# Performance work log

Hardware: AMD Instinct MI355X
Metric: run time of the kernel (lower is better)

The kernel has to match this reference:

```python
import jax, jax.numpy as jnp
import numpy as np
from jax import lax

N_QUBITS = 8
N_BLOCKS = 5

_H = jnp.array([[1.0, 1.0], [1.0, -1.0]], dtype=jnp.complex64) / np.sqrt(2.0).astype(np.float32)
# torchquantum PauliY.diagonalizing_gates = [Z, S, H] applied in order -> matrix H @ S @ Z = H @ diag(1, -1j)
_YROT = _H @ jnp.diag(jnp.array([1.0, -1j], dtype=jnp.complex64))


def apply_gate(st, U, wires):
    # st: [N, 2, 2, ..., 2] (n_qubits trailing axes); U: [2^k, 2^k]
    k = len(wires)
    axes = [w + 1 for w in wires]
    s = jnp.moveaxis(st, axes, list(range(1, k + 1)))
    shp = s.shape
    s = s.reshape(shp[0], 2 ** k, -1)
    s = jnp.einsum('ij,bjr->bir', U, s)
    return jnp.moveaxis(s.reshape(shp), list(range(1, k + 1)), axes)


def u3_mat(th, ph, lam):
    c = jnp.cos(0.5 * th).astype(jnp.complex64)
    s = jnp.sin(0.5 * th).astype(jnp.complex64)
    el = jnp.exp(1j * lam)
    ep = jnp.exp(1j * ph)
    return jnp.stack([jnp.stack([c, -el * s]), jnp.stack([ep * s, ep * el * c])])


def cu3_mat(th, ph, lam):
    M = jnp.eye(4, dtype=jnp.complex64)
    return M.at[2:, 2:].set(u3_mat(th, ph, lam))


def z_expvals(st):
    # <Z_w> for every wire from marginal probabilities
    n = st.ndim - 1
    mag = st.real ** 2 + st.imag ** 2
    outs = []
    for w in range(n):
        axes = tuple(a for a in range(1, n + 1) if a != w + 1)
        p = mag.sum(axes)  # [N, 2]
        outs.append(p[:, 0] - p[:, 1])
    return jnp.stack(outs, axis=1)


def quantum_conv(x, conv_w, conv_b, u3_params, cu3_params, fc_w, fc_b):
    n = N_QUBITS
    B, C, H, W = x.shape
    y = lax.conv_general_dilated(x, conv_w, (1, 1), 'SAME',
                                 dimension_numbers=('NCHW', 'OIHW', 'NCHW'))
    y = y + conv_b[None, :, None, None]
    ang = y.transpose(0, 2, 3, 1).reshape(-1, n)  # [B*H*W, n_qubits]
    Npx = ang.shape[0]
    # RY(theta)|0> encoding: product state of [cos(t/2), sin(t/2)] per wire
    c = jnp.cos(0.5 * ang)
    s = jnp.sin(0.5 * ang)
    st = jnp.stack([c[:, 0], s[:, 0]], axis=1).astype(jnp.complex64)
    for w in range(1, n):
        q = jnp.stack([c[:, w], s[:, w]], axis=1).astype(jnp.complex64)
        st = (st[:, :, None] * q[:, None, :]).reshape(Npx, -1)
    st = st.reshape((Npx,) + (2,) * n)
    # U3CU3Layer0: per block, U3 on each wire then circular CU3 ring
    for b in range(N_BLOCKS):
        for w in range(n):
            st = apply_gate(st, u3_mat(u3_params[b, w, 0], u3_params[b, w, 1], u3_params[b, w, 2]), [w])
        for w in range(n):
            st = apply_gate(st, cu3_mat(cu3_params[b, w, 0], cu3_params[b, w, 1], cu3_params[b, w, 2]), [w, (w + 1) % n])
    # MeasureAll(Z), then MeasureAll(X) and MeasureAll(Y) which MUTATE the device
    # state with their diagonalizing gates (torchquantum semantics)
    mz = z_expvals(st)
    for w in range(n):
        st = apply_gate(st, _H, [w])
    mx = z_expvals(st)
    for w in range(n):
        st = apply_gate(st, _YROT, [w])
    my = z_expvals(st)
    meas = jnp.concatenate([mz, mx, my], axis=1)  # [B*H*W, 3*n]
    out = meas @ fc_w.T + fc_b
    return out.reshape(B, H, W, -1).transpose(0, 3, 1, 2)


def setup_inputs() -> dict:
    key = jax.random.key(0)
    ks = jax.random.split(key, 7)
    n, cin, cout = N_QUBITS, 16, 32
    x = jax.random.normal(ks[0], (4, cin, 64, 64), dtype=jnp.float32)
    conv_w = jax.random.normal(ks[1], (n, cin, 3, 3), dtype=jnp.float32) / np.sqrt(cin * 9)
    conv_b = jax.random.normal(ks[2], (n,), dtype=jnp.float32) * 0.01
    u3_params = jax.random.uniform(ks[3], (N_BLOCKS, n, 3), dtype=jnp.float32, minval=-np.pi, maxval=np.pi)
    cu3_params = jax.random.uniform(ks[4], (N_BLOCKS, n, 3), dtype=jnp.float32, minval=-np.pi, maxval=np.pi)
    fc_w = jax.random.normal(ks[5], (cout, 3 * n), dtype=jnp.float32) / np.sqrt(3 * n)
    fc_b = jax.random.normal(ks[6], (cout,), dtype=jnp.float32) * 0.01
    return {'x': x, 'conv_w': conv_w, 'conv_b': conv_b, 'u3_params': u3_params,
            'cu3_params': cu3_params, 'fc_w': fc_w, 'fc_b': fc_b}


def reference(x, conv_w, conv_b, u3_params, cu3_params, fc_w, fc_b):
    return quantum_conv(x, conv_w, conv_b, u3_params, cu3_params, fc_w, fc_b)
```

## Files before the change

### kernel.cpp

```cpp
#include <hip/hip_runtime.h>

typedef float v2f __attribute__((ext_vector_type(2)));

template<int C>
__device__ __forceinline__ float dppmov(float x) {
  return __int_as_float(__builtin_amdgcn_update_dpp(0, __float_as_int(x), C, 0xF, 0xF, true));
}
template<int IMM>
__device__ __forceinline__ float dswz(float x) {
  return __int_as_float(__builtin_amdgcn_ds_swizzle(__float_as_int(x), IMM));
}
__device__ __forceinline__ float bperm(float x, int a) {
  return __int_as_float(__builtin_amdgcn_ds_bpermute(a, __float_as_int(x)));
}
template<int M>
__device__ __forceinline__ float bfly(float x) {
  if constexpr (M == 1)      return dppmov<0xB1>(x);
  else if constexpr (M == 2) return dppmov<0x4E>(x);
  else if constexpr (M == 3) return dppmov<0x1B>(x);
  else if constexpr (M == 8) return dppmov<0x128>(x);
  else                       return dswz<0x101F>(x);
}
template<int M>
__device__ __forceinline__ v2f bfly2(v2f v) {
  v2f o; o.x = bfly<M>(v.x); o.y = bfly<M>(v.y); return o;
}
__device__ __forceinline__ v2f sp(float s) { v2f v; v.x = s; v.y = s; return v; }
__device__ __forceinline__ v2f vfma(v2f a, v2f b, v2f c) {
  return __builtin_elementwise_fma(a, b, c);
}

template<int M, int CM>
__device__ __forceinline__ void crossG(v2f Sr[16], v2f Si[16],
    const float* __restrict__ g, int lane) {
  const bool hi = (lane & M) != 0;
  const bool ct = (lane & CM) != 0;
  float f0r = hi ? g[6]  : g[0],  f0i = hi ? g[7]  : g[1];
  float g0r = hi ? g[4]  : g[2],  g0i = hi ? g[5]  : g[3];
  float f1r = hi ? g[14] : g[8],  f1i = hi ? g[15] : g[9];
  float g1r = hi ? g[12] : g[10], g1i = hi ? g[13] : g[11];
  float fr = ct ? f1r : f0r, fi = ct ? f1i : f0i;
  float gr = ct ? g1r : g0r, gi = ct ? g1i : g0i;
  v2f vfr = sp(fr), vfi = sp(fi), vgr = sp(gr), vgi = sp(gi);
  v2f vfiN = sp(-fi), vgiN = sp(-gi);
#pragma unroll
  for (int r = 0; r < 16; ++r) {
    v2f pR = bfly2<M>(Sr[r]);
    v2f pI = bfly2<M>(Si[r]);
    v2f nR = vfma(vgiN, pI, vfma(vgr, pR, vfma(vfiN, Si[r], vfr * Sr[r])));
    v2f nI = vfma(vgi,  pR, vfma(vgr, pI, vfma(vfi,  Sr[r], vfr * Si[r])));
    Sr[r] = nR; Si[r] = nI;
  }
}

__device__ __forceinline__ void mixP(v2f& x0r, v2f& x0i, v2f& x1r, v2f& x1i,
    float m0r, float m0i, float m1r, float m1i,
    float m2r, float m2i, float m3r, float m3i) {
  v2f n0r = vfma(sp(-m1i), x1i, vfma(sp(m1r), x1r, vfma(sp(-m0i), x0i, sp(m0r) * x0r)));
  v2f n0i = vfma(sp( m1i), x1r, vfma(sp(m1r), x1i, vfma(sp( m0i), x0r, sp(m0r) * x0i)));
  v2f n1r = vfma(sp(-m3i), x1i, vfma(sp(m3r), x1r, vfma(sp(-m2i), x0i, sp(m2r) * x0r)));
  v2f n1i = vfma(sp( m3i), x1r, vfma(sp(m3r), x1i, vfma(sp( m2i), x0r, sp(m2r) * x0i)));
  x0r = n0r; x0i = n0i; x1r = n1r; x1i = n1i;
}

__device__ __forceinline__ void f4N(v2f Sr[16], v2f Si[16],
    const float* __restrict__ g, int lane) {
  const bool ct = (lane & 1) != 0;
  float m[8];
#pragma unroll
  for (int jj = 0; jj < 8; ++jj) m[jj] = ct ? g[8 + jj] : g[jj];
#pragma unroll
  for (int r = 0; r < 8; ++r)
    mixP(Sr[r], Si[r], Sr[r + 8], Si[r + 8],
         m[0], m[1], m[2], m[3], m[4], m[5], m[6], m[7]);
}
__device__ __forceinline__ void f5N(v2f Sr[16], v2f Si[16],
    const float* __restrict__ g) {
#pragma unroll
  for (int r = 0; r < 4; ++r)
    mixP(Sr[r], Si[r], Sr[r + 4], Si[r + 4],
         g[0], g[1], g[2], g[3], g[4], g[5], g[6], g[7]);
#pragma unroll
  for (int r = 8; r < 12; ++r)
    mixP(Sr[r], Si[r], Sr[r + 4], Si[r + 4],
         g[8], g[9], g[10], g[11], g[12], g[13], g[14], g[15]);
}
__device__ __forceinline__ void f67N(v2f Sr[16], v2f Si[16],
    const float* __restrict__ T) {
#pragma unroll
  for (int qd = 0; qd < 4; ++qd) {
    const int B = qd * 4;
    const float* __restrict__ M = T + (qd & 1) * 32;
    v2f ar0 = Sr[B+0], ai0 = Si[B+0], ar1 = Sr[B+1], ai1 = Si[B+1];
    v2f ar2 = Sr[B+2], ai2 = Si[B+2], ar3 = Sr[B+3], ai3 = Si[B+3];
#pragma unroll
    for (int rp = 0; rp < 4; ++rp) {
      const float* __restrict__ Mr = M + rp * 8;
      v2f nR = sp(Mr[0]) * ar0;
      nR = vfma(sp(-Mr[1]), ai0, nR);
      nR = vfma(sp( Mr[2]), ar1, nR);
      nR = vfma(sp(-Mr[3]), ai1, nR);
      nR = vfma(sp( Mr[4]), ar2, nR);
      nR = vfma(sp(-Mr[5]), ai2, nR);
      nR = vfma(sp( Mr[6]), ar3, nR);
      nR = vfma(sp(-Mr[7]), ai3, nR);
      v2f nI = sp(Mr[1]) * ar0;
      nI = vfma(sp(Mr[0]), ai0, nI);
      nI = vfma(sp(Mr[3]), ar1, nI);
      nI = vfma(sp(Mr[2]), ai1, nI);
      nI = vfma(sp(Mr[5]), ar2, nI);
      nI = vfma(sp(Mr[4]), ai2, nI);
      nI = vfma(sp(Mr[7]), ar3, nI);
      nI = vfma(sp(Mr[6]), ai3, nI);
      Sr[B + rp] = nR; Si[B + rp] = nI;
    }
  }
}
__device__ __forceinline__ void f8pN(v2f Sr[16], v2f Si[16],
    const float* __restrict__ g, int lane) {
  const bool hi = (lane & 8) != 0;
  float fr[2], fi[2], gr[2], gi[2];
  fr[0] = hi ? g[6]  : g[0];  fi[0] = hi ? g[7]  : g[1];
  gr[0] = hi ? g[4]  : g[2];  gi[0] = hi ? g[5]  : g[3];
  fr[1] = hi ? g[14] : g[8];  fi[1] = hi ? g[15] : g[9];
  gr[1] = hi ? g[12] : g[10]; gi[1] = hi ? g[13] : g[11];
#pragma unroll
  for (int r = 0; r < 16; ++r) {
    const int m = r & 1;
    v2f pR = bfly2<8>(Sr[r]);
    v2f pI = bfly2<8>(Si[r]);
    v2f nR = vfma(sp(-gi[m]), pI, vfma(sp(gr[m]), pR, vfma(sp(-fi[m]), Si[r], sp(fr[m]) * Sr[r])));
    v2f nI = vfma(sp( gi[m]), pR, vfma(sp(gr[m]), pI, vfma(sp( fi[m]), Sr[r], sp(fr[m]) * Si[r])));
    Sr[r] = nR; Si[r] = nI;
  }
}
__device__ __forceinline__ void f8N(v2f Sr[16], v2f Si[16],
    const float* __restrict__ g, int lane) {
  const bool hi = (lane & 8) != 0;
  const float fr = hi ? g[6] : g[0], fi = hi ? g[7] : g[1];
  const float gr = hi ? g[4] : g[2], gi = hi ? g[5] : g[3];
#pragma unroll
  for (int r = 1; r < 16; r += 2) {
    v2f pR = bfly2<8>(Sr[r]);
    v2f pI = bfly2<8>(Si[r]);
    v2f nR = vfma(sp(-gi), pI, vfma(sp(gr), pR, vfma(sp(-fi), Si[r], sp(fr) * Sr[r])));
    v2f nI = vfma(sp( gi), pR, vfma(sp(gr), pI, vfma(sp( fi), Sr[r], sp(fr) * Si[r])));
    Sr[r] = nR; Si[r] = nI;
  }
}

template<int M>
__device__ __forceinline__ void crossO(const v2f Sr[16], const v2f Si[16],
                                       v2f& re, v2f& im) {
  v2f r = sp(0.0f), i = sp(0.0f);
#pragma unroll
  for (int k = 0; k < 16; ++k) {
    v2f pr = bfly2<M>(Sr[k]);
    v2f pi = bfly2<M>(Si[k]);
    r = vfma(Sr[k], pr, r);
    r = vfma(Si[k], pi, r);
    i = vfma(Si[k], pr, i);
    i = vfma(-Sr[k], pi, i);
  }
  re = r; im = i;
}

__device__ __forceinline__ void mm2(const float* A, const float* B, float* D) {
  D[0] = A[0]*B[0] - A[1]*B[1] + A[2]*B[4] - A[3]*B[5];
  D[1] = A[0]*B[1] + A[1]*B[0] + A[2]*B[5] + A[3]*B[4];
  D[2] = A[0]*B[2] - A[1]*B[3] + A[2]*B[6] - A[3]*B[7];
  D[3] = A[0]*B[3] + A[1]*B[2] + A[2]*B[7] + A[3]*B[6];
  D[4] = A[4]*B[0] - A[5]*B[1] + A[6]*B[4] - A[7]*B[5];
  D[5] = A[4]*B[1] + A[5]*B[0] + A[6]*B[5] + A[7]*B[4];
  D[6] = A[4]*B[2] - A[5]*B[3] + A[6]*B[6] - A[7]*B[7];
  D[7] = A[4]*B[3] + A[5]*B[2] + A[6]*B[7] + A[7]*B[6];
}
__device__ __forceinline__ void u3fill(const float* src, float* o) {
  float th = src[0], ph = src[1], lam = src[2];
  float c = cosf(0.5f * th), s = sinf(0.5f * th);
  float cl = cosf(lam), sl = sinf(lam);
  float cp = cosf(ph), spv = sinf(ph);
  float cpl = cosf(ph + lam), spl = sinf(ph + lam);
  o[0] = c;        o[1] = 0.0f;
  o[2] = -cl * s;  o[3] = -sl * s;
  o[4] = cp * s;   o[5] = spv * s;
  o[6] = cpl * c;  o[7] = spl * c;
}

__global__ __launch_bounds__(256) void qprep_kernel(
    const float* __restrict__ u3p, const float* __restrict__ cu3p,
    const float* __restrict__ fcw, float* __restrict__ ws) {
  __shared__ float Us[40][8];
  __shared__ float Cs[40][8];
  __shared__ float Gs[640];
  const int t = threadIdx.x;
  if (t < 40) u3fill(u3p + t * 3, Us[t]);
  if (t >= 64 && t < 104) u3fill(cu3p + (t - 64) * 3, Cs[t - 64]);
  __syncthreads();
  if (t == 0) {
#pragma unroll
    for (int j = 0; j < 8; ++j) Gs[j] = Us[0][j];
  } else if (t < 36) {
    int j = t - 1, b = j / 7, k = j % 7;
    float* dst = Gs + 8 + b * 112 + k * 16;
    const float* U = Us[b * 8 + k + 1];
    const float* C = Cs[b * 8 + k];
#pragma unroll
    for (int u = 0; u < 8; ++u) dst[u] = U[u];
    mm2(C, U, dst + 8);
  } else if (t < 40) {
    int b = t - 36;
    float* dst = Gs + 568 + b * 16;
    const float* U = Us[(b + 1) * 8];
    const float* C = Cs[b * 8 + 7];
#pragma unroll
    for (int u = 0; u < 8; ++u) dst[u] = U[u];
    mm2(U, C, dst + 8);
  } else if (t == 40) {
#pragma unroll
    for (int j = 0; j < 8; ++j) Gs[632 + j] = Cs[39][j];
  }
  __syncthreads();
  if (t >= 64 && t < 104) {
    int u = t - 64;
    int b = u >> 3, idx = u & 7;
    int ct = idx >> 2, rp = idx & 3;
    const float* M6 = Gs + 8 + b * 112 + 80 + ct * 8;
    int b1p = rp >> 1, b0p = rp & 1;
    const float* M7 = Gs + 8 + b * 112 + 96 + b1p * 8;
    float* dst = ws + 1536 + b * 64 + ct * 32 + rp * 8;
#pragma unroll
    for (int c = 0; c < 4; ++c) {
      int b1 = c >> 1, b0 = c & 1;
      float a_r = M6[(b1p * 2 + b1) * 2], a_i = M6[(b1p * 2 + b1) * 2 + 1];
      float b_r = M7[(b0p * 2 + b0) * 2], b_i = M7[(b0p * 2 + b0) * 2 + 1];
      dst[c * 2]     = a_r * b_r - a_i * b_i;
      dst[c * 2 + 1] = a_r * b_i + a_i * b_r;
    }
  }
  for (int i = t; i < 32 * 28; i += 256) {
    int ch = i / 28, u = i - ch * 28;
    float v = 0.0f;
    if (u < 24) {
      float sc = (u >= 8 && (u & 7) >= 4) ? 2.0f : 1.0f;
      v = fcw[ch * 24 + u] * sc;
    }
    ws[640 + i] = v;
  }
  for (int i = t; i < 640; i += 256) ws[i] = Gs[i];
}

__global__ __launch_bounds__(256) void qconv_kernel(
    const float* __restrict__ x, const float* __restrict__ cw,
    const float* __restrict__ cb, const float* __restrict__ fcb,
    const float* __restrict__ wsc, float* __restrict__ out) {
  __shared__ float FCWs[32 * 28];
  for (int i = threadIdx.x; i < 32 * 28; i += 256) FCWs[i] = wsc[640 + i];
  __syncthreads();

  const int lane = threadIdx.x & 63;
  const int wid = __builtin_amdgcn_readfirstlane(
      (int)((blockIdx.x * blockDim.x + threadIdx.x) >> 6));
  const int p0 = wid * 8;
  const int q = lane & 15;

  float ang;
  {
    const int px = lane >> 3;
    const int oc = lane & 7;
    const int p  = p0 + px;
    const int b  = p >> 12;
    const int hh = (p >> 6) & 63;
    const int wim = p & 63;
    float acc = cb[oc];
#pragma unroll 4
    for (int ic = 0; ic < 16; ++ic) {
      const float* wp = cw + (oc * 16 + ic) * 9;
      const float* xp = x + (b * 16 + ic) * 4096;
#pragma unroll
      for (int kh = 0; kh < 3; ++kh) {
        int ih = hh + kh - 1;
        bool rok = (unsigned)ih < 64u;
        int ihc = rok ? ih : 0;
#pragma unroll
        for (int kw = 0; kw < 3; ++kw) {
          int iw = wim + kw - 1;
          bool ok = rok && ((unsigned)iw < 64u);
          int iwc = ((unsigned)iw < 64u) ? iw : 0;
          float xv = xp[ihc * 64 + iwc];
          acc = fmaf(ok ? xv : 0.0f, wp[kh * 3 + kw], acc);
        }
      }
    }
    ang = acc;
  }

  v2f Sr[16], Si[16];
  {
    const int gb = (lane & 48) << 2;
    float aA[8], aB[8];
#pragma unroll
    for (int w = 0; w < 8; ++w) {
      aA[w] = bperm(ang, gb + (w << 2));
      aB[w] = bperm(ang, gb + ((8 + w) << 2));
    }
    float cA[8], sA[8], cB[8], sB[8];
#pragma unroll
    for (int w = 0; w < 8; ++w) {
      __sincosf(0.5f * aA[w], &sA[w], &cA[w]);
      __sincosf(0.5f * aB[w], &sB[w], &cB[w]);
    }
    v2f c0; c0.x = cA[0]; c0.y = cB[0];
    v2f s0; s0.x = sA[0]; s0.y = sB[0];
    v2f c0r = vfma(sp(wsc[2]), s0, sp(wsc[0]) * c0);
    v2f c0i = vfma(sp(wsc[3]), s0, sp(wsc[1]) * c0);
    v2f s0r = vfma(sp(wsc[6]), s0, sp(wsc[4]) * c0);
    v2f s0i = vfma(sp(wsc[7]), s0, sp(wsc[5]) * c0);
    const bool w0 = (q & 8) != 0;
    v2f selR = w0 ? s0r : c0r;
    v2f selI = w0 ? s0i : c0i;
    float fA = ((q & 4) ? sA[1] : cA[1]) * ((q & 2) ? sA[2] : cA[2])
             * ((q & 1) ? sA[3] : cA[3]);
    float fB = ((q & 4) ? sB[1] : cB[1]) * ((q & 2) ? sB[2] : cB[2])
             * ((q & 1) ? sB[3] : cB[3]);
    v2f uu[4], vv[4];
    uu[0].x = cA[6]*cA[7]; uu[1].x = cA[6]*sA[7];
    uu[2].x = sA[6]*cA[7]; uu[3].x = sA[6]*sA[7];
    uu[0].y = cB[6]*cB[7]; uu[1].y = cB[6]*sB[7];
    uu[2].y = sB[6]*cB[7]; uu[3].y = sB[6]*sB[7];
    float vA0 = fA * cA[4], vA1 = fA * sA[4];
    float vB0 = fB * cB[4], vB1 = fB * sB[4];
    vv[0].x = vA0*cA[5]; vv[1].x = vA0*sA[5];
    vv[2].x = vA1*cA[5]; vv[3].x = vA1*sA[5];
    vv[0].y = vB0*cB[5]; vv[1].y = vB0*sB[5];
    vv[2].y = vB1*cB[5]; vv[3].y = vB1*sB[5];
#pragma unroll
    for (int r = 0; r < 16; ++r) {
      v2f base = vv[r >> 2] * uu[r & 3];
      Sr[r] = selR * base;
      Si[r] = selI * base;
    }
  }

  for (int b = 0; b < 5; ++b) {
    const float* __restrict__ base = wsc + 8 + b * 112;
    crossG<4, 8>(Sr, Si, base + 0, lane);
    crossG<2, 4>(Sr, Si, base + 16, lane);
    crossG<1, 2>(Sr, Si, base + 32, lane);
    f4N(Sr, Si, base + 48, lane);
    f5N(Sr, Si, base + 64);
    f67N(Sr, Si, wsc + 1536 + b * 64);
    if (b < 4) f8pN(Sr, Si, wsc + 568 + b * 16, lane);
  }
  f8N(Sr, Si, wsc + 632, lane);

  float sg[4];
  sg[0] = (q & 8) ? -1.0f : 1.0f;
  sg[1] = (q & 4) ? -1.0f : 1.0f;
  sg[2] = (q & 2) ? -1.0f : 1.0f;
  sg[3] = (q & 1) ? -1.0f : 1.0f;

  v2f PT[24];
  {
    v2f re0, im0, re1, im1, re2, im2, re3, im3;
    crossO<8>(Sr, Si, re0, im0);
    crossO<4>(Sr, Si, re1, im1);
    crossO<2>(Sr, Si, re2, im2);
    crossO<1>(Sr, Si, re3, im3);
    PT[8]  = re0; PT[9]  = re1; PT[10] = re2; PT[11] = re3;
    PT[16] = sp(sg[0]) * im0; PT[17] = sp(sg[1]) * im1;
    PT[18] = sp(sg[2]) * im2; PT[19] = sp(sg[3]) * im3;

    v2f P[16];
#pragma unroll
    for (int r = 0; r < 16; ++r) P[r] = vfma(Si[r], Si[r], Sr[r] * Sr[r]);
    v2f t01[8];
#pragma unroll
    for (int k = 0; k < 8; ++k) t01[k] = P[2*k] + P[2*k+1];
    v2f q0 = t01[0] + t01[1], q1 = t01[2] + t01[3];
    v2f q2 = t01[4] + t01[5], q3 = t01[6] + t01[7];
    v2f h0 = q0 + q1, h1 = q2 + q3;
    v2f p  = h0 + h1;
    PT[4] = h0 - h1;
    PT[5] = (q0 - q1) + (q2 - q3);
    PT[6] = (t01[0]-t01[1]) + (t01[2]-t01[3])
          + (t01[4]-t01[5]) + (t01[6]-t01[7]);
    PT[7] = (P[0]-P[1]) + (P[2]-P[3]) + (P[4]-P[5]) + (P[6]-P[7])
          + (P[8]-P[9]) + (P[10]-P[11]) + (P[12]-P[13]) + (P[14]-P[15]);
    PT[0] = sp(sg[0]) * p; PT[1] = sp(sg[1]) * p;
    PT[2] = sp(sg[2]) * p; PT[3] = sp(sg[3]) * p;

    v2f re, im;
    re = sp(0.0f); im = sp(0.0f);
#pragma unroll
    for (int r = 0; r < 8; ++r) {
      re = vfma(Sr[r], Sr[r+8], re); re = vfma(Si[r], Si[r+8], re);
      im = vfma(Si[r], Sr[r+8], im); im = vfma(-Sr[r], Si[r+8], im);
    }
    PT[12] = re; PT[20] = im;
    re = sp(0.0f); im = sp(0.0f);
#pragma unroll
    for (int t = 0; t < 8; ++t) {
      const int lo = (t & 3) + (t >> 2) * 8;
      re = vfma(Sr[lo], Sr[lo+4], re); re = vfma(Si[lo], Si[lo+4], re);
      im = vfma(Si[lo], Sr[lo+4], im); im = vfma(-Sr[lo], Si[lo+4], im);
    }
    PT[13] = re; PT[21] = im;
    re = sp(0.0f); im = sp(0.0f);
#pragma unroll
    for (int t = 0; t < 8; ++t) {
      const int lo = (t & 1) + (t >> 1) * 4;
      re = vfma(Sr[lo], Sr[lo+2], re); re = vfma(Si[lo], Si[lo+2], re);
      im = vfma(Si[lo], Sr[lo+2], im); im = vfma(-Sr[lo], Si[lo+2], im);
    }
    PT[14] = re; PT[22] = im;
    re = sp(0.0f); im = sp(0.0f);
#pragma unroll
    for (int t = 0; t < 8; ++t) {
      const int lo = 2 * t;
      re = vfma(Sr[lo], Sr[lo+1], re); re = vfma(Si[lo], Si[lo+1], re);
      im = vfma(Si[lo], Sr[lo+1], im); im = vfma(-Sr[lo], Si[lo+1], im);
    }
    PT[15] = re; PT[23] = im;
  }

  const int j = q & 7;
  const bool isB = (q & 8) != 0;
  float mm[24];
#pragma unroll
  for (int t = 0; t < 24; ++t) {
    v2f v = PT[t] + bfly2<8>(PT[t]);
    float s = isB ? v.y : v.x;
    s += bfly<1>(s);
    s += bfly<2>(s);
    s += bfly<4>(s);
    mm[t] = s;
  }

  const int g = lane >> 4;
  const int p = p0 + 2 * g + (isB ? 1 : 0);
  const int ob = (p >> 12) * 131072 + (p & 4095);
#pragma unroll
  for (int k = 0; k < 4; ++k) {
    const int ch = 4 * j + k;
    const float* wr = FCWs + ch * 28;
    float acc = fcb[ch];
#pragma unroll
    for (int u = 0; u < 24; ++u) acc = fmaf(mm[u], wr[u], acc);
    out[ob + ch * 4096] = acc;
  }
}

extern "C" void kernel_launch(void* const* d_in, const int* in_sizes, int n_in,
                              void* d_out, int out_size, void* d_ws, size_t ws_size,
                              hipStream_t stream) {
  const float* x      = (const float*)d_in[0];
  const float* conv_w = (const float*)d_in[1];
  const float* conv_b = (const float*)d_in[2];
  const float* u3p    = (const float*)d_in[3];
  const float* cu3p   = (const float*)d_in[4];
  const float* fcw    = (const float*)d_in[5];
  const float* fcb    = (const float*)d_in[6];
  float* out = (float*)d_out;
  float* ws  = (float*)d_ws;

  qprep_kernel<<<1, 256, 0, stream>>>(u3p, cu3p, fcw, ws);
  qconv_kernel<<<512, 256, 0, stream>>>(x, conv_w, conv_b, fcb, ws, out);
}
```

Baseline: 112.7 us.

## Fuse gate-prep kernel into main kernel and read gate matrices from LDS

```diff
diff --git a/kernel.cpp b/kernel.cpp
--- a/kernel.cpp
+++ b/kernel.cpp
@@ -5,10 +5,6 @@
 template<int C>
 __device__ __forceinline__ float dppmov(float x) {
   return __int_as_float(__builtin_amdgcn_update_dpp(0, __float_as_int(x), C, 0xF, 0xF, true));
-}
-template<int IMM>
-__device__ __forceinline__ float dswz(float x) {
-  return __int_as_float(__builtin_amdgcn_ds_swizzle(__float_as_int(x), IMM));
 }
 __device__ __forceinline__ float bperm(float x, int a) {
   return __int_as_float(__builtin_amdgcn_ds_bpermute(a, __float_as_int(x)));
@@ -19,7 +15,7 @@
   else if constexpr (M == 2) return dppmov<0x4E>(x);
   else if constexpr (M == 3) return dppmov<0x1B>(x);
   else if constexpr (M == 8) return dppmov<0x128>(x);
-  else                       return dswz<0x101F>(x);
+  else                       return dppmov<0x1B>(dppmov<0x141>(x));
 }
 template<int M>
 __device__ __forceinline__ v2f bfly2(v2f v) {
@@ -32,7 +28,7 @@
 
 template<int M, int CM>
 __device__ __forceinline__ void crossG(v2f Sr[16], v2f Si[16],
-    const float* __restrict__ g, int lane) {
+    const float* g, int lane) {
   const bool hi = (lane & M) != 0;
   const bool ct = (lane & CM) != 0;
   float f0r = hi ? g[6]  : g[0],  f0i = hi ? g[7]  : g[1];
@@ -64,7 +60,7 @@
 }
 
 __device__ __forceinline__ void f4N(v2f Sr[16], v2f Si[16],
-    const float* __restrict__ g, int lane) {
+    const float* g, int lane) {
   const bool ct = (lane & 1) != 0;
   float m[8];
 #pragma unroll
@@ -74,8 +70,7 @@
     mixP(Sr[r], Si[r], Sr[r + 8], Si[r + 8],
          m[0], m[1], m[2], m[3], m[4], m[5], m[6], m[7]);
 }
-__device__ __forceinline__ void f5N(v2f Sr[16], v2f Si[16],
-    const float* __restrict__ g) {
+__device__ __forceinline__ void f5N(v2f Sr[16], v2f Si[16], const float* g) {
 #pragma unroll
   for (int r = 0; r < 4; ++r)
     mixP(Sr[r], Si[r], Sr[r + 4], Si[r + 4],
@@ -85,17 +80,16 @@
     mixP(Sr[r], Si[r], Sr[r + 4], Si[r + 4],
          g[8], g[9], g[10], g[11], g[12], g[13], g[14], g[15]);
 }
-__device__ __forceinline__ void f67N(v2f Sr[16], v2f Si[16],
-    const float* __restrict__ T) {
+__device__ __forceinline__ void f67N(v2f Sr[16], v2f Si[16], const float* T) {
 #pragma unroll
   for (int qd = 0; qd < 4; ++qd) {
     const int B = qd * 4;
-    const float* __restrict__ M = T + (qd & 1) * 32;
+    const float* M = T + (qd & 1) * 32;
     v2f ar0 = Sr[B+0], ai0 = Si[B+0], ar1 = Sr[B+1], ai1 = Si[B+1];
     v2f ar2 = Sr[B+2], ai2 = Si[B+2], ar3 = Sr[B+3], ai3 = Si[B+3];
 #pragma unroll
     for (int rp = 0; rp < 4; ++rp) {
-      const float* __restrict__ Mr = M + rp * 8;
+      const float* Mr = M + rp * 8;
       v2f nR = sp(Mr[0]) * ar0;
       nR = vfma(sp(-Mr[1]), ai0, nR);
       nR = vfma(sp( Mr[2]), ar1, nR);
@@ -117,7 +111,7 @@
   }
 }
 __device__ __forceinline__ void f8pN(v2f Sr[16], v2f Si[16],
-    const float* __restrict__ g, int lane) {
+    const float* g, int lane) {
   const bool hi = (lane & 8) != 0;
   float fr[2], fi[2], gr[2], gi[2];
   fr[0] = hi ? g[6]  : g[0];  fi[0] = hi ? g[7]  : g[1];
@@ -135,7 +129,7 @@
   }
 }
 __device__ __forceinline__ void f8N(v2f Sr[16], v2f Si[16],
-    const float* __restrict__ g, int lane) {
+    const float* g, int lane) {
   const bool hi = (lane & 8) != 0;
   const float fr = hi ? g[6] : g[0], fi = hi ? g[7] : g[1];
   const float gr = hi ? g[4] : g[2], gi = hi ? g[5] : g[3];
@@ -187,76 +181,74 @@
   o[6] = cpl * c;  o[7] = spl * c;
 }
 
-__global__ __launch_bounds__(256) void qprep_kernel(
-    const float* __restrict__ u3p, const float* __restrict__ cu3p,
-    const float* __restrict__ fcw, float* __restrict__ ws) {
+__global__ __launch_bounds__(256) void qconv_kernel(
+    const float* __restrict__ x, const float* __restrict__ cw,
+    const float* __restrict__ cb, const float* __restrict__ u3p,
+    const float* __restrict__ cu3p, const float* __restrict__ fcw,
+    const float* __restrict__ fcb, float* __restrict__ out) {
   __shared__ float Us[40][8];
   __shared__ float Cs[40][8];
   __shared__ float Gs[640];
-  const int t = threadIdx.x;
-  if (t < 40) u3fill(u3p + t * 3, Us[t]);
-  if (t >= 64 && t < 104) u3fill(cu3p + (t - 64) * 3, Cs[t - 64]);
-  __syncthreads();
-  if (t == 0) {
-#pragma unroll
-    for (int j = 0; j < 8; ++j) Gs[j] = Us[0][j];
-  } else if (t < 36) {
-    int j = t - 1, b = j / 7, k = j % 7;
-    float* dst = Gs + 8 + b * 112 + k * 16;
-    const float* U = Us[b * 8 + k + 1];
-    const float* C = Cs[b * 8 + k];
-#pragma unroll
-    for (int u = 0; u < 8; ++u) dst[u] = U[u];
-    mm2(C, U, dst + 8);
-  } else if (t < 40) {
-    int b = t - 36;
-    float* dst = Gs + 568 + b * 16;
-    const float* U = Us[(b + 1) * 8];
-    const float* C = Cs[b * 8 + 7];
-#pragma unroll
-    for (int u = 0; u < 8; ++u) dst[u] = U[u];
-    mm2(U, C, dst + 8);
-  } else if (t == 40) {
-#pragma unroll
-    for (int j = 0; j < 8; ++j) Gs[632 + j] = Cs[39][j];
-  }
-  __syncthreads();
-  if (t >= 64 && t < 104) {
-    int u = t - 64;
-    int b = u >> 3, idx = u & 7;
-    int ct = idx >> 2, rp = idx & 3;
-    const float* M6 = Gs + 8 + b * 112 + 80 + ct * 8;
-    int b1p = rp >> 1, b0p = rp & 1;
-    const float* M7 = Gs + 8 + b * 112 + 96 + b1p * 8;
-    float* dst = ws + 1536 + b * 64 + ct * 32 + rp * 8;
-#pragma unroll
-    for (int c = 0; c < 4; ++c) {
-      int b1 = c >> 1, b0 = c & 1;
-      float a_r = M6[(b1p * 2 + b1) * 2], a_i = M6[(b1p * 2 + b1) * 2 + 1];
-      float b_r = M7[(b0p * 2 + b0) * 2], b_i = M7[(b0p * 2 + b0) * 2 + 1];
-      dst[c * 2]     = a_r * b_r - a_i * b_i;
-      dst[c * 2 + 1] = a_r * b_i + a_i * b_r;
-    }
-  }
-  for (int i = t; i < 32 * 28; i += 256) {
-    int ch = i / 28, u = i - ch * 28;
-    float v = 0.0f;
-    if (u < 24) {
-      float sc = (u >= 8 && (u & 7) >= 4) ? 2.0f : 1.0f;
-      v = fcw[ch * 24 + u] * sc;
-    }
-    ws[640 + i] = v;
-  }
-  for (int i = t; i < 640; i += 256) ws[i] = Gs[i];
-}
-
-__global__ __launch_bounds__(256) void qconv_kernel(
-    const float* __restrict__ x, const float* __restrict__ cw,
-    const float* __restrict__ cb, const float* __restrict__ fcb,
-    const float* __restrict__ wsc, float* __restrict__ out) {
-  __shared__ float FCWs[32 * 28];
-  for (int i = threadIdx.x; i < 32 * 28; i += 256) FCWs[i] = wsc[640 + i];
-  __syncthreads();
+  __shared__ float FCWs[32 * 29];
+  __shared__ float F67t[320];
+
+  {
+    const int t = threadIdx.x;
+    if (t < 40) u3fill(u3p + t * 3, Us[t]);
+    if (t >= 64 && t < 104) u3fill(cu3p + (t - 64) * 3, Cs[t - 64]);
+    for (int i = t; i < 32 * 29; i += 256) {
+      int ch = i / 29, u = i - ch * 29;
+      float v = 0.0f;
+      if (u < 24) {
+        float sc = (u >= 8 && (u & 7) >= 4) ? 2.0f : 1.0f;
+        v = fcw[ch * 24 + u] * sc;
+      }
+      FCWs[i] = v;
+    }
+    __syncthreads();
+    if (t == 0) {
+#pragma unroll
+      for (int j = 0; j < 8; ++j) Gs[j] = Us[0][j];
+    } else if (t < 36) {
+      int j = t - 1, b = j / 7, k = j % 7;
+      float* dst = Gs + 8 + b * 112 + k * 16;
+      const float* U = Us[b * 8 + k + 1];
+      const float* C = Cs[b * 8 + k];
+#pragma unroll
+      for (int u = 0; u < 8; ++u) dst[u] = U[u];
+      mm2(C, U, dst + 8);
+    } else if (t < 40) {
+      int b = t - 36;
+      float* dst = Gs + 568 + b * 16;
+      const float* U = Us[(b + 1) * 8];
+      const float* C = Cs[b * 8 + 7];
+#pragma unroll
+      for (int u = 0; u < 8; ++u) dst[u] = U[u];
+      mm2(U, C, dst + 8);
+    } else if (t == 40) {
+#pragma unroll
+      for (int j = 0; j < 8; ++j) Gs[632 + j] = Cs[39][j];
+    }
+    __syncthreads();
+    if (t >= 64 && t < 104) {
+      int u = t - 64;
+      int b = u >> 3, idx = u & 7;
+      int ct = idx >> 2, rp = idx & 3;
+      const float* M6 = Gs + 8 + b * 112 + 80 + ct * 8;
+      int b1p = rp >> 1, b0p = rp & 1;
+      const float* M7 = Gs + 8 + b * 112 + 96 + b1p * 8;
+      float* dst = F67t + b * 64 + ct * 32 + rp * 8;
+#pragma unroll
+      for (int c = 0; c < 4; ++c) {
+        int b1 = c >> 1, b0 = c & 1;
+        float a_r = M6[(b1p * 2 + b1) * 2], a_i = M6[(b1p * 2 + b1) * 2 + 1];
+        float b_r = M7[(b0p * 2 + b0) * 2], b_i = M7[(b0p * 2 + b0) * 2 + 1];
+        dst[c * 2]     = a_r * b_r - a_i * b_i;
+        dst[c * 2 + 1] = a_r * b_i + a_i * b_r;
+      }
+    }
+    __syncthreads();
+  }
 
   const int lane = threadIdx.x & 63;
   const int wid = __builtin_amdgcn_readfirstlane(
@@ -312,10 +304,10 @@
     }
     v2f c0; c0.x = cA[0]; c0.y = cB[0];
     v2f s0; s0.x = sA[0]; s0.y = sB[0];
-    v2f c0r = vfma(sp(wsc[2]), s0, sp(wsc[0]) * c0);
-    v2f c0i = vfma(sp(wsc[3]), s0, sp(wsc[1]) * c0);
-    v2f s0r = vfma(sp(wsc[6]), s0, sp(wsc[4]) * c0);
-    v2f s0i = vfma(sp(wsc[7]), s0, sp(wsc[5]) * c0);
+    v2f c0r = vfma(sp(Gs[2]), s0, sp(Gs[0]) * c0);
+    v2f c0i = vfma(sp(Gs[3]), s0, sp(Gs[1]) * c0);
+    v2f s0r = vfma(sp(Gs[6]), s0, sp(Gs[4]) * c0);
+    v2f s0i = vfma(sp(Gs[7]), s0, sp(Gs[5]) * c0);
     const bool w0 = (q & 8) != 0;
     v2f selR = w0 ? s0r : c0r;
     v2f selI = w0 ? s0i : c0i;
@@ -343,16 +335,16 @@
   }
 
   for (int b = 0; b < 5; ++b) {
-    const float* __restrict__ base = wsc + 8 + b * 112;
+    const float* base = Gs + 8 + b * 112;
     crossG<4, 8>(Sr, Si, base + 0, lane);
     crossG<2, 4>(Sr, Si, base + 16, lane);
     crossG<1, 2>(Sr, Si, base + 32, lane);
     f4N(Sr, Si, base + 48, lane);
     f5N(Sr, Si, base + 64);
-    f67N(Sr, Si, wsc + 1536 + b * 64);
-    if (b < 4) f8pN(Sr, Si, wsc + 568 + b * 16, lane);
-  }
-  f8N(Sr, Si, wsc + 632, lane);
+    f67N(Sr, Si, F67t + b * 64);
+    if (b < 4) f8pN(Sr, Si, Gs + 568 + b * 16, lane);
+  }
+  f8N(Sr, Si, Gs + 632, lane);
 
   float sg[4];
   sg[0] = (q & 8) ? -1.0f : 1.0f;
@@ -443,7 +435,7 @@
 #pragma unroll
   for (int k = 0; k < 4; ++k) {
     const int ch = 4 * j + k;
-    const float* wr = FCWs + ch * 28;
+    const float* wr = FCWs + ch * 29;
     float acc = fcb[ch];
 #pragma unroll
     for (int u = 0; u < 24; ++u) acc = fmaf(mm[u], wr[u], acc);
@@ -462,8 +454,7 @@
   const float* fcw    = (const float*)d_in[5];
   const float* fcb    = (const float*)d_in[6];
   float* out = (float*)d_out;
-  float* ws  = (float*)d_ws;
-
-  qprep_kernel<<<1, 256, 0, stream>>>(u3p, cu3p, fcw, ws);
-  qconv_kernel<<<512, 256, 0, stream>>>(x, conv_w, conv_b, fcb, ws, out);
-}
+
+  qconv_kernel<<<512, 256, 0, stream>>>(x, conv_w, conv_b, u3p, cu3p,
+                                        fcw, fcb, out);
+}
```

Result: faster. 108.1 us (-4.1%).
